# Performance work log

Hardware: AMD Instinct MI355X
Metric: run time of the kernel (lower is better)

Reference implementation:

```python
import jax, jax.numpy as jnp
import numpy as np

B = 1_000_000
N_DIR, N_TRIAL = 2, 4
ALPHA, R_GAS, EPS = 0.3, 8.314462618, 1e-12
TAU_CLIP, LN_CLIP = 10.0, 20.0
EPS_FD, SIGMA, MARGIN = 1e-4, 0.05, 0.0
LAM_PHY, LAM_GD, LAM_TPD = 1.0, 0.1, 0.1


def renorm3(x):
    # clamp to >=0 and normalize so components sum to 1 (last axis)
    x = jnp.maximum(x, 0.0)
    return x / jnp.maximum(x.sum(-1, keepdims=True), EPS)


def nrtl_ln_gamma(x, T, g):
    # x: (B,3), T: (B,), g: (B,3,3) -> ln_gamma: (B,3)
    x = jnp.maximum(x, 0.0)
    Tc = jnp.maximum(T, 1.0)
    tau = jnp.clip(g / (R_GAS * jnp.maximum(Tc, EPS)[:, None, None]), -TAU_CLIP, TAU_CLIP)
    G = jnp.exp(-ALPHA * tau)
    denom = jnp.maximum(jnp.einsum('bj,bji->bi', x, G), EPS)          # (B,3)
    A = jnp.einsum('bj,bji->bi', x, tau * G)                          # (B,3), == num1 in torch
    term1 = A / denom
    W = x[:, None, :] * G / denom[:, None, :]                         # (B,3,3)
    inside = tau - (A / denom)[:, None, :]
    term2 = (W * inside).sum(-1)
    return jnp.clip(term1 + term2, -LN_CLIP, LN_CLIP)


def setup_inputs() -> dict:
    key = jax.random.key(0)
    k1, k2, k3, k4, k5, k6 = jax.random.split(key, 6)
    pred = jax.random.uniform(k1, (B, 6), dtype=jnp.float32, minval=0.01, maxval=1.0)
    target = jax.random.uniform(k2, (B, 6), dtype=jnp.float32, minval=0.01, maxval=1.0)
    T = 298.0 + 100.0 * jax.random.uniform(k3, (B,), dtype=jnp.float32)  # Kelvin
    g = 800.0 * jax.random.normal(k4, (B, 3, 3), dtype=jnp.float32)      # J/mol
    # simplex directions: zero-sum, unit-norm (matches _sample_simplex_directions)
    v = jax.random.normal(k5, (N_DIR, B, 3), dtype=jnp.float32)
    v = v - v.mean(-1, keepdims=True)
    dirs = v / jnp.maximum(jnp.linalg.norm(v, axis=-1, keepdims=True), 1e-12)
    noise = SIGMA * jax.random.normal(k6, (N_TRIAL, B, 3), dtype=jnp.float32)
    return {'pred': pred, 'target': target, 'T': T, 'g': g, 'dirs': dirs, 'noise': noise}


def reference(pred, target, T, g, dirs, noise):
    # supervised MSE on (E+R) compositions
    L_sup = jnp.mean((pred - target) ** 2)

    xE = renorm3(pred[:, :3])
    xR = renorm3(pred[:, 3:])
    ln_gE = nrtl_ln_gamma(xE, T, g)
    ln_gR = nrtl_ln_gamma(xR, T, g)
    # chemical potential residual r_k = ln(xE_k gE_k) - ln(xR_k gR_k)
    r = jnp.log(jnp.maximum(xE, EPS)) + ln_gE - (jnp.log(jnp.maximum(xR, EPS)) + ln_gR)
    L_phy = jnp.mean(r ** 2)

    lg = jax.vmap(lambda xx: nrtl_ln_gamma(xx, T, g))  # over trial/direction axis

    # Gibbs-Duhem finite-difference penalty along simplex directions
    x_p = renorm3(xE[None] + EPS_FD * dirs)            # (N_DIR,B,3)
    x_m = renorm3(xE[None] - EPS_FD * dirs)
    d_ln = (lg(x_p) - lg(x_m)) / (2.0 * EPS_FD)
    gd = (xE[None] * d_ln).sum(-1)                     # (N_DIR,B)
    L_gd = jnp.mean(gd * gd)

    # TPD stability penalty
    w = renorm3(xE[None] + noise)                      # (N_TRIAL,B,3)
    ln_gw = lg(w)
    tpd = (w * (jnp.log(jnp.maximum(w, EPS)) + ln_gw
                - jnp.log(jnp.maximum(xE, EPS))[None] - ln_gE[None])).sum(-1)
    L_tpd = jnp.mean(jnp.maximum(MARGIN - tpd, 0.0))

    return L_sup + LAM_PHY * L_phy + LAM_GD * L_gd + LAM_TPD * L_tpd
```

## Files before the change

### kernel.cpp

```cpp
#include <hip/hip_runtime.h>


constexpr float ALPHA    = 0.3f;
constexpr float R_GAS    = 8.314462618f;
constexpr float EPS      = 1e-12f;
constexpr float TAU_CLIP = 10.0f;
constexpr float LN_CLIP  = 20.0f;
constexpr float EPS_FD   = 1e-4f;

constexpr float LOG2E = 1.44269504088896340736f;
constexpr float LN2   = 0.69314718055994530942f;

typedef float v2f __attribute__((ext_vector_type(2)));

__device__ __forceinline__ float clipf(float v, float lo, float hi) {
    return fminf(fmaxf(v, lo), hi);
}
__device__ __forceinline__ float fast_rcp(float x) { return __builtin_amdgcn_rcpf(x); }
__device__ __forceinline__ v2f nt_load2(const float* p) {
    return __builtin_nontemporal_load((const v2f*)p);
}
__device__ __forceinline__ float nt_load(const float* p) {
    return __builtin_nontemporal_load(p);
}

struct Mats {
    float tau[3][3];
    float G[3][3];
    float tG[3][3];
};

__device__ __forceinline__ void ln_gamma3(const float x[3], const Mats& M, float lg[3]) {
    float ratio[3], c[3];
#pragma unroll
    for (int i = 0; i < 3; ++i) {
        float d = x[0] * M.G[0][i] + x[1] * M.G[1][i] + x[2] * M.G[2][i];
        d = fmaxf(d, EPS);
        float A = x[0] * M.tG[0][i] + x[1] * M.tG[1][i] + x[2] * M.tG[2][i];
        float inv = fast_rcp(d);
        ratio[i] = A * inv;
        c[i] = x[i] * inv;
    }
#pragma unroll
    for (int i = 0; i < 3; ++i) {
        float s = ratio[i];
#pragma unroll
        for (int j = 0; j < 3; ++j) {
            s += c[j] * (M.tG[i][j] - M.G[i][j] * ratio[j]);
        }
        lg[i] = clipf(s, -LN_CLIP, LN_CLIP);
    }
}

__device__ __forceinline__ void renorm3(float x[3]) {
    x[0] = fmaxf(x[0], 0.0f);
    x[1] = fmaxf(x[1], 0.0f);
    x[2] = fmaxf(x[2], 0.0f);
    float inv = fast_rcp(fmaxf(x[0] + x[1] + x[2], EPS));
    x[0] *= inv; x[1] *= inv; x[2] *= inv;
}

__global__ __launch_bounds__(256, 4) void nrtl_loss_kernel(
    const float* __restrict__ pred,
    const float* __restrict__ target,
    const float* __restrict__ Tarr,
    const float* __restrict__ g,
    const float* __restrict__ dirs,
    const float* __restrict__ noise,
    float* __restrict__ partials, int B)
{
    const int i = blockIdx.x * blockDim.x + threadIdx.x;
    float contrib = 0.0f;

    if (i < B) {
        const float* prow = pred   + (size_t)i * 6;
        const float* trow = target + (size_t)i * 6;
        const float* grow = g      + (size_t)i * 9;

        v2f p01 = nt_load2(prow);
        v2f p23 = nt_load2(prow + 2);
        v2f p45 = nt_load2(prow + 4);
        v2f t01 = nt_load2(trow);
        v2f t23 = nt_load2(trow + 2);
        v2f t45 = nt_load2(trow + 4);
        float Tv = nt_load(Tarr + i);
        float gv[9];
#pragma unroll
        for (int k = 0; k < 9; ++k) gv[k] = nt_load(grow + k);
        float dv[2][3];
#pragma unroll
        for (int d = 0; d < 2; ++d) {
            const float* drow = dirs + ((size_t)d * B + i) * 3;
#pragma unroll
            for (int k = 0; k < 3; ++k) dv[d][k] = nt_load(drow + k);
        }
        float nv[4][3];
#pragma unroll
        for (int tr = 0; tr < 4; ++tr) {
            const float* nrow = noise + ((size_t)tr * B + i) * 3;
#pragma unroll
            for (int k = 0; k < 3; ++k) nv[tr][k] = nt_load(nrow + k);
        }

        float sup;
        {
            float d0 = p01.x - t01.x, d1 = p01.y - t01.y;
            float d2 = p23.x - t23.x, d3 = p23.y - t23.y;
            float d4 = p45.x - t45.x, d5 = p45.y - t45.y;
            sup = d0 * d0 + d1 * d1 + d2 * d2 + d3 * d3 + d4 * d4 + d5 * d5;
        }

        float xE[3] = {p01.x, p01.y, p23.x};
        float xR[3] = {p23.y, p45.x, p45.y};
        renorm3(xE);
        renorm3(xR);

        const float Tc = fmaxf(Tv, 1.0f);
        const float invRT = fast_rcp(R_GAS * Tc);
        Mats M;
#pragma unroll
        for (int a = 0; a < 3; ++a) {
#pragma unroll
            for (int b = 0; b < 3; ++b) {
                float ta = clipf(gv[a * 3 + b] * invRT, -TAU_CLIP, TAU_CLIP);
                float Gv = __builtin_amdgcn_exp2f((-ALPHA * LOG2E) * ta);
                M.tau[a][b] = ta;
                M.G[a][b]   = Gv;
                M.tG[a][b]  = ta * Gv;
            }
        }

        float lgE[3], lgR[3];
        ln_gamma3(xE, M, lgE);
        ln_gamma3(xR, M, lgR);

        float logxE[3];
        float phy = 0.0f;
#pragma unroll
        for (int k = 0; k < 3; ++k) {
            logxE[k] = LN2 * __builtin_amdgcn_logf(fmaxf(xE[k], EPS));
            float logxR = LN2 * __builtin_amdgcn_logf(fmaxf(xR[k], EPS));
            float r = logxE[k] + lgE[k] - logxR - lgR[k];
            phy += r * r;
        }

        float gdsum = 0.0f;
#pragma unroll
        for (int d = 0; d < 2; ++d) {
            float xp[3], xm[3];
#pragma unroll
            for (int k = 0; k < 3; ++k) {
                xp[k] = xE[k] + EPS_FD * dv[d][k];
                xm[k] = xE[k] - EPS_FD * dv[d][k];
            }
            renorm3(xp);
            renorm3(xm);
            float lgp[3], lgm[3];
            ln_gamma3(xp, M, lgp);
            ln_gamma3(xm, M, lgm);
            float gd = 0.0f;
#pragma unroll
            for (int k = 0; k < 3; ++k) gd += xE[k] * (lgp[k] - lgm[k]);
            gd *= 0.5f / EPS_FD;
            gdsum += gd * gd;
        }

        float base[3];
#pragma unroll
        for (int k = 0; k < 3; ++k) base[k] = logxE[k] + lgE[k];

        float tpdsum = 0.0f;
#pragma unroll
        for (int tr = 0; tr < 4; ++tr) {
            float w[3];
#pragma unroll
            for (int k = 0; k < 3; ++k) w[k] = xE[k] + nv[tr][k];
            renorm3(w);
            float lgw[3];
            ln_gamma3(w, M, lgw);
            float tpd = 0.0f;
#pragma unroll
            for (int k = 0; k < 3; ++k) {
                float logw = LN2 * __builtin_amdgcn_logf(fmaxf(w[k], EPS));
                tpd += w[k] * (logw + lgw[k] - base[k]);
            }
            tpdsum += fmaxf(-tpd, 0.0f);
        }

        const float invB = 1.0f / (float)B;
        contrib = invB * (sup * (1.0f / 6.0f)
                          + phy * (1.0f / 3.0f)
                          + 0.05f * gdsum
                          + 0.025f * tpdsum);
    }

#pragma unroll
    for (int off = 32; off > 0; off >>= 1)
        contrib += __shfl_down(contrib, off, 64);

    __shared__ float ssum[4];
    const int lane = threadIdx.x & 63;
    const int wid  = threadIdx.x >> 6;
    if (lane == 0) ssum[wid] = contrib;
    __syncthreads();
    if (threadIdx.x == 0) {
        partials[blockIdx.x] = ssum[0] + ssum[1] + ssum[2] + ssum[3];
    }
}

__global__ __launch_bounds__(256) void reduce_kernel(
    const float* __restrict__ partials, int n, float* __restrict__ out)
{
    double sacc = 0.0;
    for (int j = threadIdx.x; j < n; j += 256) sacc += (double)partials[j];
#pragma unroll
    for (int off = 32; off > 0; off >>= 1)
        sacc += __shfl_down(sacc, off, 64);
    __shared__ double ds[4];
    const int lane = threadIdx.x & 63;
    const int wid  = threadIdx.x >> 6;
    if (lane == 0) ds[wid] = sacc;
    __syncthreads();
    if (threadIdx.x == 0) out[0] = (float)(ds[0] + ds[1] + ds[2] + ds[3]);
}

extern "C" void kernel_launch(void* const* d_in, const int* in_sizes, int n_in,
                              void* d_out, int out_size, void* d_ws, size_t ws_size,
                              hipStream_t stream) {
    const float* pred   = (const float*)d_in[0];
    const float* target = (const float*)d_in[1];
    const float* Tarr   = (const float*)d_in[2];
    const float* g      = (const float*)d_in[3];
    const float* dirs   = (const float*)d_in[4];
    const float* noise  = (const float*)d_in[5];
    const int B = in_sizes[2];

    float* partials = (float*)d_ws;
    float* out      = (float*)d_out;

    const int block = 256;
    const int grid  = (B + block - 1) / block;
    nrtl_loss_kernel<<<grid, block, 0, stream>>>(pred, target, Tarr, g, dirs, noise, partials, B);
    reduce_kernel<<<1, block, 0, stream>>>(partials, grid, out);
}
```

Before: 169.3 us.

## Process two rows per thread with packed v2f math and wider loads

```diff
diff --git a/kernel.cpp b/kernel.cpp
--- a/kernel.cpp
+++ b/kernel.cpp
@@ -12,55 +12,72 @@
 constexpr float LN2   = 0.69314718055994530942f;
 
 typedef float v2f __attribute__((ext_vector_type(2)));
-
-__device__ __forceinline__ float clipf(float v, float lo, float hi) {
-    return fminf(fmaxf(v, lo), hi);
-}
-__device__ __forceinline__ float fast_rcp(float x) { return __builtin_amdgcn_rcpf(x); }
+typedef float v4f __attribute__((ext_vector_type(4)));
+
+__device__ __forceinline__ v2f make2(float s) { return (v2f){s, s}; }
+__device__ __forceinline__ v2f pk_rcp(v2f a) {
+    return (v2f){__builtin_amdgcn_rcpf(a.x), __builtin_amdgcn_rcpf(a.y)};
+}
+__device__ __forceinline__ v2f pk_exp2(v2f a) {
+    return (v2f){__builtin_amdgcn_exp2f(a.x), __builtin_amdgcn_exp2f(a.y)};
+}
+__device__ __forceinline__ v2f pk_ln(v2f a) {
+    return make2(LN2) * (v2f){__builtin_amdgcn_logf(fmaxf(a.x, EPS)),
+                              __builtin_amdgcn_logf(fmaxf(a.y, EPS))};
+}
+__device__ __forceinline__ v2f pk_max(v2f a, v2f b) { return __builtin_elementwise_max(a, b); }
+__device__ __forceinline__ v2f pk_min(v2f a, v2f b) { return __builtin_elementwise_min(a, b); }
+__device__ __forceinline__ v2f pk_clip(v2f v, float lo, float hi) {
+    return pk_min(pk_max(v, make2(lo)), make2(hi));
+}
+
 __device__ __forceinline__ v2f nt_load2(const float* p) {
     return __builtin_nontemporal_load((const v2f*)p);
 }
+__device__ __forceinline__ v4f nt_load4(const float* p) {
+    return __builtin_nontemporal_load((const v4f*)p);
+}
 __device__ __forceinline__ float nt_load(const float* p) {
     return __builtin_nontemporal_load(p);
 }
 
-struct Mats {
-    float tau[3][3];
-    float G[3][3];
-    float tG[3][3];
+struct MatsP {
+    v2f tau[3][3];
+    v2f G[3][3];
+    v2f tG[3][3];
 };
 
-__device__ __forceinline__ void ln_gamma3(const float x[3], const Mats& M, float lg[3]) {
-    float ratio[3], c[3];
+__device__ __forceinline__ void ln_gamma3p(const v2f x[3], const MatsP& M, v2f lg[3]) {
+    v2f ratio[3], c[3];
 #pragma unroll
     for (int i = 0; i < 3; ++i) {
-        float d = x[0] * M.G[0][i] + x[1] * M.G[1][i] + x[2] * M.G[2][i];
-        d = fmaxf(d, EPS);
-        float A = x[0] * M.tG[0][i] + x[1] * M.tG[1][i] + x[2] * M.tG[2][i];
-        float inv = fast_rcp(d);
+        v2f d = x[0] * M.G[0][i] + x[1] * M.G[1][i] + x[2] * M.G[2][i];
+        d = pk_max(d, make2(EPS));
+        v2f A = x[0] * M.tG[0][i] + x[1] * M.tG[1][i] + x[2] * M.tG[2][i];
+        v2f inv = pk_rcp(d);
         ratio[i] = A * inv;
         c[i] = x[i] * inv;
     }
 #pragma unroll
     for (int i = 0; i < 3; ++i) {
-        float s = ratio[i];
+        v2f s = ratio[i];
 #pragma unroll
         for (int j = 0; j < 3; ++j) {
             s += c[j] * (M.tG[i][j] - M.G[i][j] * ratio[j]);
         }
-        lg[i] = clipf(s, -LN_CLIP, LN_CLIP);
-    }
-}
-
-__device__ __forceinline__ void renorm3(float x[3]) {
-    x[0] = fmaxf(x[0], 0.0f);
-    x[1] = fmaxf(x[1], 0.0f);
-    x[2] = fmaxf(x[2], 0.0f);
-    float inv = fast_rcp(fmaxf(x[0] + x[1] + x[2], EPS));
+        lg[i] = pk_clip(s, -LN_CLIP, LN_CLIP);
+    }
+}
+
+__device__ __forceinline__ void renorm3p(v2f x[3]) {
+    x[0] = pk_max(x[0], make2(0.0f));
+    x[1] = pk_max(x[1], make2(0.0f));
+    x[2] = pk_max(x[2], make2(0.0f));
+    v2f inv = pk_rcp(pk_max(x[0] + x[1] + x[2], make2(EPS)));
     x[0] *= inv; x[1] *= inv; x[2] *= inv;
 }
 
-__global__ __launch_bounds__(256, 4) void nrtl_loss_kernel(
+__global__ __launch_bounds__(256) void nrtl_loss_kernel(
     const float* __restrict__ pred,
     const float* __restrict__ target,
     const float* __restrict__ Tarr,
@@ -69,129 +86,147 @@
     const float* __restrict__ noise,
     float* __restrict__ partials, int B)
 {
-    const int i = blockIdx.x * blockDim.x + threadIdx.x;
-    float contrib = 0.0f;
-
-    if (i < B) {
-        const float* prow = pred   + (size_t)i * 6;
-        const float* trow = target + (size_t)i * 6;
-        const float* grow = g      + (size_t)i * 9;
-
-        v2f p01 = nt_load2(prow);
-        v2f p23 = nt_load2(prow + 2);
-        v2f p45 = nt_load2(prow + 4);
-        v2f t01 = nt_load2(trow);
-        v2f t23 = nt_load2(trow + 2);
-        v2f t45 = nt_load2(trow + 4);
-        float Tv = nt_load(Tarr + i);
-        float gv[9];
-#pragma unroll
-        for (int k = 0; k < 9; ++k) gv[k] = nt_load(grow + k);
-        float dv[2][3];
-#pragma unroll
-        for (int d = 0; d < 2; ++d) {
-            const float* drow = dirs + ((size_t)d * B + i) * 3;
-#pragma unroll
-            for (int k = 0; k < 3; ++k) dv[d][k] = nt_load(drow + k);
-        }
-        float nv[4][3];
-#pragma unroll
-        for (int tr = 0; tr < 4; ++tr) {
-            const float* nrow = noise + ((size_t)tr * B + i) * 3;
-#pragma unroll
-            for (int k = 0; k < 3; ++k) nv[tr][k] = nt_load(nrow + k);
-        }
-
-        float sup;
-        {
-            float d0 = p01.x - t01.x, d1 = p01.y - t01.y;
-            float d2 = p23.x - t23.x, d3 = p23.y - t23.y;
-            float d4 = p45.x - t45.x, d5 = p45.y - t45.y;
-            sup = d0 * d0 + d1 * d1 + d2 * d2 + d3 * d3 + d4 * d4 + d5 * d5;
-        }
-
-        float xE[3] = {p01.x, p01.y, p23.x};
-        float xR[3] = {p23.y, p45.x, p45.y};
-        renorm3(xE);
-        renorm3(xR);
-
-        const float Tc = fmaxf(Tv, 1.0f);
-        const float invRT = fast_rcp(R_GAS * Tc);
-        Mats M;
+    const int  tix = blockIdx.x * blockDim.x + threadIdx.x;
+    const long i0  = (long)tix * 2;
+    float contrib  = 0.0f;
+
+    if (i0 < B) {
+        const bool full = (i0 + 1 < B);
+
+        v2f p[6], tt[6], gk[9], Tv2;
+        if (full) {
+            const float* pr = pred + (size_t)i0 * 6;
+            v4f P0 = nt_load4(pr), P1 = nt_load4(pr + 4), P2 = nt_load4(pr + 8);
+            p[0] = (v2f){P0.x, P1.z}; p[1] = (v2f){P0.y, P1.w}; p[2] = (v2f){P0.z, P2.x};
+            p[3] = (v2f){P0.w, P2.y}; p[4] = (v2f){P1.x, P2.z}; p[5] = (v2f){P1.y, P2.w};
+            const float* trp = target + (size_t)i0 * 6;
+            v4f T0 = nt_load4(trp), T1 = nt_load4(trp + 4), T2 = nt_load4(trp + 8);
+            tt[0] = (v2f){T0.x, T1.z}; tt[1] = (v2f){T0.y, T1.w}; tt[2] = (v2f){T0.z, T2.x};
+            tt[3] = (v2f){T0.w, T2.y}; tt[4] = (v2f){T1.x, T2.z}; tt[5] = (v2f){T1.y, T2.w};
+            Tv2 = nt_load2(Tarr + i0);
+            const float* gr = g + (size_t)i0 * 9;
+            v2f c0 = nt_load2(gr),      c1 = nt_load2(gr + 2),  c2 = nt_load2(gr + 4);
+            v2f c3 = nt_load2(gr + 6),  c4 = nt_load2(gr + 8),  c5 = nt_load2(gr + 10);
+            v2f c6 = nt_load2(gr + 12), c7 = nt_load2(gr + 14), c8 = nt_load2(gr + 16);
+            gk[0] = (v2f){c0.x, c4.y}; gk[1] = (v2f){c0.y, c5.x}; gk[2] = (v2f){c1.x, c5.y};
+            gk[3] = (v2f){c1.y, c6.x}; gk[4] = (v2f){c2.x, c6.y}; gk[5] = (v2f){c2.y, c7.x};
+            gk[6] = (v2f){c3.x, c7.y}; gk[7] = (v2f){c3.y, c8.x}; gk[8] = (v2f){c4.x, c8.y};
+        } else {
+            const float* pr  = pred   + (size_t)i0 * 6;
+            const float* trp = target + (size_t)i0 * 6;
+            const float* gr  = g      + (size_t)i0 * 9;
+#pragma unroll
+            for (int k = 0; k < 6; ++k) { p[k] = make2(nt_load(pr + k)); tt[k] = make2(nt_load(trp + k)); }
+            Tv2 = make2(nt_load(Tarr + i0));
+#pragma unroll
+            for (int k = 0; k < 9; ++k) gk[k] = make2(nt_load(gr + k));
+        }
+
+        v2f sup = make2(0.0f);
+#pragma unroll
+        for (int k = 0; k < 6; ++k) { v2f d = p[k] - tt[k]; sup += d * d; }
+
+        v2f xE[3] = {p[0], p[1], p[2]};
+        v2f xR[3] = {p[3], p[4], p[5]};
+        renorm3p(xE);
+        renorm3p(xR);
+
+        v2f Tc    = pk_max(Tv2, make2(1.0f));
+        v2f invRT = pk_rcp(make2(R_GAS) * Tc);
+        MatsP M;
 #pragma unroll
         for (int a = 0; a < 3; ++a) {
 #pragma unroll
             for (int b = 0; b < 3; ++b) {
-                float ta = clipf(gv[a * 3 + b] * invRT, -TAU_CLIP, TAU_CLIP);
-                float Gv = __builtin_amdgcn_exp2f((-ALPHA * LOG2E) * ta);
+                v2f ta = pk_clip(gk[a * 3 + b] * invRT, -TAU_CLIP, TAU_CLIP);
+                v2f Gv = pk_exp2(make2(-ALPHA * LOG2E) * ta);
                 M.tau[a][b] = ta;
                 M.G[a][b]   = Gv;
                 M.tG[a][b]  = ta * Gv;
             }
         }
 
-        float lgE[3], lgR[3];
-        ln_gamma3(xE, M, lgE);
-        ln_gamma3(xR, M, lgR);
-
-        float logxE[3];
-        float phy = 0.0f;
+        v2f lgE[3], lgR[3];
+        ln_gamma3p(xE, M, lgE);
+        ln_gamma3p(xR, M, lgR);
+
+        v2f logxE[3];
+        v2f phy = make2(0.0f);
 #pragma unroll
         for (int k = 0; k < 3; ++k) {
-            logxE[k] = LN2 * __builtin_amdgcn_logf(fmaxf(xE[k], EPS));
-            float logxR = LN2 * __builtin_amdgcn_logf(fmaxf(xR[k], EPS));
-            float r = logxE[k] + lgE[k] - logxR - lgR[k];
+            logxE[k]  = pk_ln(xE[k]);
+            v2f logxR = pk_ln(xR[k]);
+            v2f r = logxE[k] + lgE[k] - logxR - lgR[k];
             phy += r * r;
         }
 
-        float gdsum = 0.0f;
+        v2f gdsum = make2(0.0f);
 #pragma unroll
         for (int d = 0; d < 2; ++d) {
-            float xp[3], xm[3];
+            v2f dv[3];
+            const float* dr = dirs + ((size_t)d * B + i0) * 3;
+            if (full) {
+                v2f a = nt_load2(dr), b = nt_load2(dr + 2), c = nt_load2(dr + 4);
+                dv[0] = (v2f){a.x, b.y}; dv[1] = (v2f){a.y, c.x}; dv[2] = (v2f){b.x, c.y};
+            } else {
+#pragma unroll
+                for (int k = 0; k < 3; ++k) dv[k] = make2(nt_load(dr + k));
+            }
+            v2f xp[3], xm[3];
 #pragma unroll
             for (int k = 0; k < 3; ++k) {
-                xp[k] = xE[k] + EPS_FD * dv[d][k];
-                xm[k] = xE[k] - EPS_FD * dv[d][k];
-            }
-            renorm3(xp);
-            renorm3(xm);
-            float lgp[3], lgm[3];
-            ln_gamma3(xp, M, lgp);
-            ln_gamma3(xm, M, lgm);
-            float gd = 0.0f;
+                xp[k] = xE[k] + make2(EPS_FD) * dv[k];
+                xm[k] = xE[k] - make2(EPS_FD) * dv[k];
+            }
+            renorm3p(xp);
+            renorm3p(xm);
+            v2f lgp[3], lgm[3];
+            ln_gamma3p(xp, M, lgp);
+            ln_gamma3p(xm, M, lgm);
+            v2f gd = make2(0.0f);
 #pragma unroll
             for (int k = 0; k < 3; ++k) gd += xE[k] * (lgp[k] - lgm[k]);
-            gd *= 0.5f / EPS_FD;
+            gd *= make2(0.5f / EPS_FD);
             gdsum += gd * gd;
         }
 
-        float base[3];
+        v2f base[3];
 #pragma unroll
         for (int k = 0; k < 3; ++k) base[k] = logxE[k] + lgE[k];
 
-        float tpdsum = 0.0f;
+        v2f tpdsum = make2(0.0f);
 #pragma unroll
         for (int tr = 0; tr < 4; ++tr) {
-            float w[3];
-#pragma unroll
-            for (int k = 0; k < 3; ++k) w[k] = xE[k] + nv[tr][k];
-            renorm3(w);
-            float lgw[3];
-            ln_gamma3(w, M, lgw);
-            float tpd = 0.0f;
+            v2f nv[3];
+            const float* nr = noise + ((size_t)tr * B + i0) * 3;
+            if (full) {
+                v2f a = nt_load2(nr), b = nt_load2(nr + 2), c = nt_load2(nr + 4);
+                nv[0] = (v2f){a.x, b.y}; nv[1] = (v2f){a.y, c.x}; nv[2] = (v2f){b.x, c.y};
+            } else {
+#pragma unroll
+                for (int k = 0; k < 3; ++k) nv[k] = make2(nt_load(nr + k));
+            }
+            v2f w[3];
+#pragma unroll
+            for (int k = 0; k < 3; ++k) w[k] = xE[k] + nv[k];
+            renorm3p(w);
+            v2f lgw[3];
+            ln_gamma3p(w, M, lgw);
+            v2f tpd = make2(0.0f);
 #pragma unroll
             for (int k = 0; k < 3; ++k) {
-                float logw = LN2 * __builtin_amdgcn_logf(fmaxf(w[k], EPS));
+                v2f logw = pk_ln(w[k]);
                 tpd += w[k] * (logw + lgw[k] - base[k]);
             }
-            tpdsum += fmaxf(-tpd, 0.0f);
+            tpdsum += pk_max(-tpd, make2(0.0f));
         }
 
         const float invB = 1.0f / (float)B;
-        contrib = invB * (sup * (1.0f / 6.0f)
-                          + phy * (1.0f / 3.0f)
-                          + 0.05f * gdsum
-                          + 0.025f * tpdsum);
+        v2f c2 = (sup * make2(1.0f / 6.0f)
+                  + phy * make2(1.0f / 3.0f)
+                  + make2(0.05f)  * gdsum
+                  + make2(0.025f) * tpdsum) * make2(invB);
+        contrib = full ? (c2.x + c2.y) : c2.x;
     }
 
 #pragma unroll
@@ -239,7 +274,8 @@
     float* out      = (float*)d_out;
 
     const int block = 256;
-    const int grid  = (B + block - 1) / block;
+    const int pairs = (B + 1) / 2;
+    const int grid  = (pairs + block - 1) / block;
     nrtl_loss_kernel<<<grid, block, 0, stream>>>(pred, target, Tarr, g, dirs, noise, partials, B);
     reduce_kernel<<<1, block, 0, stream>>>(partials, grid, out);
 }
```

Result: slower. 183.9 us (+8.6%).
